# Kernel tuning notes

Measured on AMD Instinct MI355X. Metric: run time of the kernel, lower is better.

The kernel has to match this reference:

```python
import jax, jax.numpy as jnp
import numpy as np

N, DEG, F, H, OUT = 50000, 16, 128, 128, 64


def _lstm_aggr(neigh, w_ih, w_hh, b_ih, b_hh):
    # neigh: [N, D, F] fixed-degree neighbor features; run LSTM over D steps,
    # return final hidden state [N, H] (PyG SAGEConv 'lstm' aggregation).
    n, d, f = neigh.shape
    h_dim = w_hh.shape[1]

    def step(carry, xt):
        h, c = carry
        gates = xt @ w_ih.T + b_ih + h @ w_hh.T + b_hh  # [N, 4H]
        i, fg, g, o = jnp.split(gates, 4, axis=-1)      # torch gate order i,f,g,o
        i = jax.nn.sigmoid(i)
        fg = jax.nn.sigmoid(fg)
        g = jnp.tanh(g)
        o = jax.nn.sigmoid(o)
        c = fg * c + i * g
        h = o * jnp.tanh(c)
        return (h, c), None

    h0 = jnp.zeros((n, h_dim), neigh.dtype)
    (h, _), _ = jax.lax.scan(step, (h0, h0), jnp.swapaxes(neigh, 0, 1))
    return h


def _sage_lstm(x, src, w_ih, w_hh, b_ih, b_hh, wl, bl, wr):
    # SAGEConv: out = lin_l(lstm_aggr(x[neighbors])) + lin_r(x)
    neigh = x[src]                                   # [N, D, F] gather
    aggr = _lstm_aggr(neigh, w_ih, w_hh, b_ih, b_hh)  # [N, H]
    return aggr @ wl.T + bl + x @ wr.T


def setup_inputs() -> dict:
    key = jax.random.key(0)
    ks = jax.random.split(key, 16)
    x = jax.random.normal(ks[0], (N, F), dtype=jnp.float32)
    # fixed-degree graph: dst = arange(N) each repeated DEG times (sorted, as
    # PyG lstm aggregation requires), src random -> edge_index [2, N*DEG]
    src = jax.random.randint(ks[1], (N * DEG,), 0, N, dtype=jnp.int64)
    dst = jnp.repeat(jnp.arange(N, dtype=jnp.int64), DEG)
    edge_index = jnp.stack([src, dst])
    s = 1.0 / np.sqrt(H)
    def u(k, shape):
        return jax.random.uniform(k, shape, jnp.float32, -s, s)
    params = {
        # layer 1 (input F -> hidden H)
        "w_ih1": u(ks[2], (4 * H, F)), "w_hh1": u(ks[3], (4 * H, H)),
        "b_ih1": u(ks[4], (4 * H,)), "b_hh1": u(ks[5], (4 * H,)),
        "lin_l1_w": u(ks[6], (H, H)), "lin_l1_b": u(ks[6], (H,)),
        "lin_r1_w": u(ks[7], (H, F)),
        # layer 2 (H -> H)
        "w_ih2": u(ks[8], (4 * H, H)), "w_hh2": u(ks[9], (4 * H, H)),
        "b_ih2": u(ks[10], (4 * H,)), "b_hh2": u(ks[11], (4 * H,)),
        "lin_l2_w": u(ks[12], (H, H)), "lin_l2_b": u(ks[12], (H,)),
        "lin_r2_w": u(ks[13], (H, H)),
        # output head
        "lin_w": u(ks[14], (OUT, H)), "lin_b": u(ks[15], (OUT,)),
    }
    return {"x": x, "edge_index": edge_index, **params}


def reference(x, edge_index,
              w_ih1, w_hh1, b_ih1, b_hh1, lin_l1_w, lin_l1_b, lin_r1_w,
              w_ih2, w_hh2, b_ih2, b_hh2, lin_l2_w, lin_l2_b, lin_r2_w,
              lin_w, lin_b):
    n = x.shape[0]
    deg = edge_index.shape[1] // n
    src = edge_index[0].reshape(n, deg)  # fixed-degree neighbor matrix
    h = _sage_lstm(x, src, w_ih1, w_hh1, b_ih1, b_hh1, lin_l1_w, lin_l1_b, lin_r1_w)
    h = jax.nn.relu(h)
    h = _sage_lstm(h, src, w_ih2, w_hh2, b_ih2, b_hh2, lin_l2_w, lin_l2_b, lin_r2_w)
    h = jax.nn.relu(h)
    return h @ lin_w.T + lin_b
```

## Files before the change

### kernel.cpp

```cpp
#include <hip/hip_runtime.h>
#include <stdint.h>

#define NN 50000
#define DEG 16
#define MT 32
#define NBLK ((NN + MT - 1) / MT)
#define LOG2E 1.4426950408889634f

typedef short bf16x8 __attribute__((ext_vector_type(8)));
typedef float f32x4 __attribute__((ext_vector_type(4)));
typedef unsigned short u16;
typedef unsigned int u32;

static __device__ __forceinline__ u16 f2bf(float f) {
  union { float f; u32 u; } v; v.f = f;
  u32 u = v.u + 0x7FFFu + ((v.u >> 16) & 1u);
  return (u16)(u >> 16);
}
static __device__ __forceinline__ float rcp_(float x) {
  return __builtin_amdgcn_rcpf(x);
}
static __device__ __forceinline__ float ex2_(float x) {
  return __builtin_amdgcn_exp2f(x);
}
static __device__ __forceinline__ void gload_lds16(const void* g, void* l) {
  __builtin_amdgcn_global_load_lds(
      (const __attribute__((address_space(1))) void*)g,
      (__attribute__((address_space(3))) void*)l, 16, 0, 0);
}

__global__ void k_prep(const float* __restrict__ x, u16* __restrict__ xb,
                       const float* __restrict__ wih1, const float* __restrict__ whh1, u16* __restrict__ wpk1,
                       const float* __restrict__ wih2, const float* __restrict__ whh2, u16* __restrict__ wpk2,
                       const float* __restrict__ lr1, const float* __restrict__ ll1, u16* __restrict__ epk1,
                       const float* __restrict__ lr2, const float* __restrict__ ll2, u16* __restrict__ epk2,
                       const float* __restrict__ linw, u16* __restrict__ hpk,
                       const float* __restrict__ bi1, const float* __restrict__ bh1, float* __restrict__ bs1,
                       const float* __restrict__ bi2, const float* __restrict__ bh2, float* __restrict__ bs2) {
  int b = blockIdx.x;
  if (b < 128) {
    const float* wih = (b < 64) ? wih1 : wih2;
    const float* whh = (b < 64) ? whh1 : whh2;
    u16* wpk = (b < 64) ? wpk1 : wpk2;
    int t = (b & 63) * 256 + threadIdx.x;
    int lane = t & 63, kt = (t >> 6) & 7, g = (t >> 9) & 3, w = (t >> 11) & 7;
    int col = g * 128 + w * 16 + (lane & 15);
    int k0 = kt * 32 + (lane >> 4) * 8;
    float sc = (g == 2) ? 2.f * LOG2E : LOG2E;
#pragma unroll
    for (int j = 0; j < 8; ++j) {
      int k = k0 + j;
      float v = (k < 128) ? wih[col * 128 + k] : whh[col * 128 + k - 128];
      wpk[t * 8 + j] = f2bf(sc * v);
    }
  } else if (b < 160) {
    const float* lrw = (b < 144) ? lr1 : lr2;
    const float* llw = (b < 144) ? ll1 : ll2;
    u16* epk = (b < 144) ? epk1 : epk2;
    int t = ((b - 128) & 15) * 256 + threadIdx.x;
    int lane = t & 63, kt = (t >> 6) & 7, w = (t >> 9) & 7;
    int col = w * 16 + (lane & 15);
    int k0 = kt * 32 + (lane >> 4) * 8;
#pragma unroll
    for (int j = 0; j < 8; ++j) {
      int k = k0 + j;
      epk[t * 8 + j] = f2bf(k < 128 ? lrw[col * 128 + k] : llw[col * 128 + k - 128]);
    }
  } else if (b < 164) {
    int t = (b - 160) * 256 + threadIdx.x;
    int lane = t & 63, kt = (t >> 6) & 3, w = (t >> 8) & 3;
    int col = w * 16 + (lane & 15);
    int k0 = kt * 32 + (lane >> 4) * 8;
#pragma unroll
    for (int j = 0; j < 8; ++j) hpk[t * 8 + j] = f2bf(linw[col * 128 + k0 + j]);
  } else if (b < 168) {
    int t = (b - 164) * 256 + threadIdx.x;
    if (t < 1024) {
      int i = t & 511;
      float sc = ((i >> 7) == 2) ? 2.f * LOG2E : LOG2E;
      if (t < 512) bs1[i] = sc * (bi1[i] + bh1[i]);
      else bs2[i] = sc * (bi2[i] + bh2[i]);
    }
  } else {
    int i = (b - 168) * 256 + threadIdx.x;
    int stride = (gridDim.x - 168) * 256;
    for (; i < NN * 128 / 4; i += stride) {
      float4 v = ((const float4*)x)[i];
      ushort4 o;
      o.x = f2bf(v.x); o.y = f2bf(v.y); o.z = f2bf(v.z); o.w = f2bf(v.w);
      ((ushort4*)xb)[i] = o;
    }
  }
}


#define GATHER(DCODE, PDST)                                                   \
  do {                                                                        \
    int idx_;                                                                 \
    if ((DCODE) < DEG) idx_ = IDX[grow * DEG + (DCODE)];                      \
    else idx_ = (node0 + grow < NN) ? node0 + grow : NN - 1;                  \
    const char* gsw_ = (const char*)(xin + (size_t)idx_ * 128) +              \
                       ((lr * 16) ^ ((grow & 15) << 4));                      \
    gload_lds16(gsw_, (PDST) + (w * 4) * 128);                                \
  } while (0)

#define CBAR(N)                                                               \
  do {                                                                        \
    asm volatile("s_waitcnt vmcnt(" #N ") lgkmcnt(0)" ::: "memory");          \
    __builtin_amdgcn_s_barrier();                                             \
    __builtin_amdgcn_sched_barrier(0);                                        \
  } while (0)

template <int L2>
__global__ __launch_bounds__(512, 2) void k_layer(
    const u16* __restrict__ xin, const int* __restrict__ src,
    const u16* __restrict__ wpk, const float* __restrict__ bsum,
    const u16* __restrict__ epk, const float* __restrict__ linlb,
    u16* __restrict__ hout, const u16* __restrict__ hpk,
    const float* __restrict__ linb, float* __restrict__ dout) {
  __shared__ __align__(16) u16 AX[3][MT * 128];
  __shared__ __align__(16) u16 AH[2][MT * 128];
  __shared__ int IDX[MT * DEG];

  const int tid = threadIdx.x;
  const int w = tid >> 6, l = tid & 63;
  const int lr = l & 15, lh = l >> 4;
  const int node0 = blockIdx.x * MT;
  const int grow = w * 4 + lh;

  bf16x8 wreg[4][8];
#pragma unroll
  for (int g = 0; g < 4; ++g)
#pragma unroll
    for (int kt = 0; kt < 8; ++kt)
      wreg[g][kt] = *(const bf16x8*)(wpk + (size_t)(((w * 4 + g) * 8 + kt) * 64 + l) * 8);

  IDX[tid] = (node0 + (tid >> 4) < NN) ? src[node0 * DEG + tid] : 0;

  float gb[4];
#pragma unroll
  for (int g = 0; g < 4; ++g) gb[g] = bsum[g * 128 + w * 16 + lr];
  float eb = linlb[w * 16 + lr];
  __syncthreads();

  GATHER(0, AX[0]);
  GATHER(1, AX[1]);

  f32x4 c[2];
  c[0] = (f32x4){0.f, 0.f, 0.f, 0.f};
  c[1] = (f32x4){0.f, 0.f, 0.f, 0.f};
  CBAR(1);

  u16 *pA = AX[0], *pB = AX[1], *pC = AX[2];

#pragma unroll 1
  for (int step = 0; step < DEG; ++step) {
    const int cb = step & 1, nb = cb ^ 1;

    if (step < DEG - 1) GATHER(step + 2, pC);

    f32x4 acc[2][4];
#pragma unroll
    for (int mt = 0; mt < 2; ++mt)
#pragma unroll
      for (int g = 0; g < 4; ++g)
        acc[mt][g] = (f32x4){gb[g], gb[g], gb[g], gb[g]};

#pragma unroll
    for (int kt = 0; kt < 4; ++kt) {
      bf16x8 af[2];
#pragma unroll
      for (int mt = 0; mt < 2; ++mt) {
        int row = mt * 16 + lr;
        af[mt] = *(const bf16x8*)((const char*)pA + row * 256 +
                                  ((kt * 64 + lh * 16) ^ ((row & 15) << 4)));
      }
#pragma unroll
      for (int g = 0; g < 4; ++g)
#pragma unroll
        for (int mt = 0; mt < 2; ++mt)
          acc[mt][g] = __builtin_amdgcn_mfma_f32_16x16x32_bf16(af[mt], wreg[g][kt], acc[mt][g], 0, 0, 0);
    }

    if (step) {
#pragma unroll
      for (int kt = 0; kt < 4; ++kt) {
        bf16x8 af[2];
#pragma unroll
        for (int mt = 0; mt < 2; ++mt) {
          int row = mt * 16 + lr;
          af[mt] = *(const bf16x8*)((const char*)AH[cb] + row * 256 +
                                    ((kt * 64 + lh * 16) ^ ((row & 15) << 4)));
        }
#pragma unroll
        for (int g = 0; g < 4; ++g)
#pragma unroll
          for (int mt = 0; mt < 2; ++mt)
            acc[mt][g] = __builtin_amdgcn_mfma_f32_16x16x32_bf16(af[mt], wreg[g][4 + kt], acc[mt][g], 0, 0, 0);
      }
    }

#pragma unroll
    for (int mt = 0; mt < 2; ++mt)
#pragma unroll
      for (int r = 0; r < 4; ++r) {
        float iv = rcp_(1.f + ex2_(-acc[mt][0][r]));
        float fv = rcp_(1.f + ex2_(-acc[mt][1][r]));
        float gv = 1.f - 2.f * rcp_(1.f + ex2_(acc[mt][2][r]));
        float ov = rcp_(1.f + ex2_(-acc[mt][3][r]));
        float cv = fv * c[mt][r] + iv * gv;
        c[mt][r] = cv;
        float th = 1.f - 2.f * rcp_(1.f + ex2_(2.f * LOG2E * cv));
        int row = mt * 16 + lh * 4 + r;
        int jj = 2 * (w * 16 + lr);
        *(u16*)((char*)AH[nb] + row * 256 + (jj ^ ((row & 15) << 4))) =
            f2bf(ov * th);
      }

    if (step < DEG - 1) CBAR(1);
    else CBAR(0);

    u16* t_ = pA; pA = pB; pB = t_; 
    t_ = pB; pB = pC; pC = t_;
  }

  f32x4 eacc[2];
  eacc[0] = (f32x4){eb, eb, eb, eb};
  eacc[1] = (f32x4){eb, eb, eb, eb};
#pragma unroll
  for (int kt = 0; kt < 8; ++kt) {
    const u16* srcb = (kt < 4) ? pA : AH[0];
    int kb = (kt & 3) * 64 + lh * 16;
    bf16x8 af[2];
#pragma unroll
    for (int mt = 0; mt < 2; ++mt) {
      int row = mt * 16 + lr;
      af[mt] = *(const bf16x8*)((const char*)srcb + row * 256 +
                                (kb ^ ((row & 15) << 4)));
    }
    bf16x8 bf = *(const bf16x8*)(epk + (size_t)((w * 8 + kt) * 64 + l) * 8);
#pragma unroll
    for (int mt = 0; mt < 2; ++mt)
      eacc[mt] = __builtin_amdgcn_mfma_f32_16x16x32_bf16(af[mt], bf, eacc[mt], 0, 0, 0);
  }

  if constexpr (!L2) {
#pragma unroll
    for (int mt = 0; mt < 2; ++mt)
#pragma unroll
      for (int r = 0; r < 4; ++r) {
        int node = node0 + mt * 16 + lh * 4 + r;
        if (node < NN) {
          float v = fmaxf(eacc[mt][r], 0.f);
          hout[(size_t)node * 128 + w * 16 + lr] = f2bf(v);
        }
      }
  } else {
#pragma unroll
    for (int mt = 0; mt < 2; ++mt)
#pragma unroll
      for (int r = 0; r < 4; ++r) {
        int row = mt * 16 + lh * 4 + r;
        float v = fmaxf(eacc[mt][r], 0.f);
        int jj = 2 * (w * 16 + lr);
        *(u16*)((char*)AH[1] + row * 256 + (jj ^ ((row & 15) << 4))) = f2bf(v);
      }
    __syncthreads();
    if (w < 4) {
      float hb = linb[w * 16 + lr];
      f32x4 hacc[2];
      hacc[0] = (f32x4){hb, hb, hb, hb};
      hacc[1] = (f32x4){hb, hb, hb, hb};
#pragma unroll
      for (int kt = 0; kt < 4; ++kt) {
        bf16x8 af[2];
#pragma unroll
        for (int mt = 0; mt < 2; ++mt) {
          int row = mt * 16 + lr;
          af[mt] = *(const bf16x8*)((const char*)AH[1] + row * 256 +
                                    ((kt * 64 + lh * 16) ^ ((row & 15) << 4)));
        }
        bf16x8 bf = *(const bf16x8*)(hpk + (size_t)((w * 4 + kt) * 64 + l) * 8);
#pragma unroll
        for (int mt = 0; mt < 2; ++mt)
          hacc[mt] = __builtin_amdgcn_mfma_f32_16x16x32_bf16(af[mt], bf, hacc[mt], 0, 0, 0);
      }
#pragma unroll
      for (int mt = 0; mt < 2; ++mt)
#pragma unroll
        for (int r = 0; r < 4; ++r) {
          int node = node0 + mt * 16 + lh * 4 + r;
          if (node < NN) dout[(size_t)node * 64 + w * 16 + lr] = hacc[mt][r];
        }
    }
  }
}

extern "C" void kernel_launch(void* const* d_in, const int* in_sizes, int n_in,
                              void* d_out, int out_size, void* d_ws, size_t ws_size,
                              hipStream_t stream) {
  const float* x    = (const float*)d_in[0];
  const int*   edge = (const int*)d_in[1];
  const float* wih1 = (const float*)d_in[2];
  const float* whh1 = (const float*)d_in[3];
  const float* bih1 = (const float*)d_in[4];
  const float* bhh1 = (const float*)d_in[5];
  const float* ll1w = (const float*)d_in[6];
  const float* ll1b = (const float*)d_in[7];
  const float* lr1w = (const float*)d_in[8];
  const float* wih2 = (const float*)d_in[9];
  const float* whh2 = (const float*)d_in[10];
  const float* bih2 = (const float*)d_in[11];
  const float* bhh2 = (const float*)d_in[12];
  const float* ll2w = (const float*)d_in[13];
  const float* ll2b = (const float*)d_in[14];
  const float* lr2w = (const float*)d_in[15];
  const float* linw = (const float*)d_in[16];
  const float* linb = (const float*)d_in[17];

  char* ws = (char*)d_ws;
  u16* xb    = (u16*)(ws);
  u16* h1b   = (u16*)(ws + 12800000);
  u16* wpk1  = (u16*)(ws + 25600000);
  u16* wpk2  = (u16*)(ws + 25862144);
  u16* epk1  = (u16*)(ws + 26124288);
  u16* epk2  = (u16*)(ws + 26189824);
  u16* hpk   = (u16*)(ws + 26255360);
  float* bs1 = (float*)(ws + 26271744);
  float* bs2 = (float*)(ws + 26273792);

  k_prep<<<1000, 256, 0, stream>>>(x, xb,
                                   wih1, whh1, wpk1, wih2, whh2, wpk2,
                                   lr1w, ll1w, epk1, lr2w, ll2w, epk2,
                                   linw, hpk,
                                   bih1, bhh1, bs1, bih2, bhh2, bs2);
  k_layer<0><<<NBLK, 512, 0, stream>>>(xb, edge, wpk1, bs1, epk1, ll1b,
                                       h1b, nullptr, nullptr, nullptr);
  k_layer<1><<<NBLK, 512, 0, stream>>>(h1b, edge, wpk2, bs2, epk2, ll2b,
                                       nullptr, hpk, linb, (float*)d_out);
}
```

Baseline: 530.0 us.

## Load gathered neighbor rows directly into registers with 16-node tiles

Reduces the node tile from 32 to 16 rows per block. Gathered neighbor features now go straight from global memory into MFMA operand registers instead of through a triple-buffered LDS staging area. The input-projection MFMAs for the next step are interleaved with the recurrent step, and s_setprio is added around MFMA bursts. This drops LDS traffic and the vmcnt waits, and doubles the block count for occupancy and latency hiding. In exchange each block has more barrier and per-step overhead and reuses each weight-register load over half as many rows. The bounds checks are removed because 50000 divides evenly by 16.

```diff
diff --git a/kernel.cpp b/kernel.cpp
--- a/kernel.cpp
+++ b/kernel.cpp
@@ -3,7 +3,7 @@
 
 #define NN 50000
 #define DEG 16
-#define MT 32
+#define MT 16
 #define NBLK ((NN + MT - 1) / MT)
 #define LOG2E 1.4426950408889634f
 
@@ -22,11 +22,6 @@
 }
 static __device__ __forceinline__ float ex2_(float x) {
   return __builtin_amdgcn_exp2f(x);
-}
-static __device__ __forceinline__ void gload_lds16(const void* g, void* l) {
-  __builtin_amdgcn_global_load_lds(
-      (const __attribute__((address_space(1))) void*)g,
-      (__attribute__((address_space(3))) void*)l, 16, 0, 0);
 }
 
 __global__ void k_prep(const float* __restrict__ x, u16* __restrict__ xb,
@@ -94,19 +89,30 @@
 }
 
 
-#define GATHER(DCODE, PDST)                                                   \
+#define XLOAD(DCODE)                                                          \
   do {                                                                        \
-    int idx_;                                                                 \
-    if ((DCODE) < DEG) idx_ = IDX[grow * DEG + (DCODE)];                      \
-    else idx_ = (node0 + grow < NN) ? node0 + grow : NN - 1;                  \
-    const char* gsw_ = (const char*)(xin + (size_t)idx_ * 128) +              \
-                       ((lr * 16) ^ ((grow & 15) << 4));                      \
-    gload_lds16(gsw_, (PDST) + (w * 4) * 128);                                \
+    int idx_ = ((DCODE) < DEG) ? IDXT[(DCODE) * 16 + lr] : node0 + lr;        \
+    const u16* b_ = xin + (size_t)idx_ * 128 + lh * 8;                        \
+    xf[0] = *(const bf16x8*)(b_);                                             \
+    xf[1] = *(const bf16x8*)(b_ + 32);                                        \
+    xf[2] = *(const bf16x8*)(b_ + 64);                                        \
+    xf[3] = *(const bf16x8*)(b_ + 96);                                        \
   } while (0)
 
-#define CBAR(N)                                                               \
+#define XPART()                                                               \
   do {                                                                        \
-    asm volatile("s_waitcnt vmcnt(" #N ") lgkmcnt(0)" ::: "memory");          \
+    __builtin_amdgcn_s_setprio(1);                                            \
+    _Pragma("unroll") for (int g = 0; g < 4; ++g)                             \
+        acc[g] = (f32x4){gb[g], gb[g], gb[g], gb[g]};                         \
+    _Pragma("unroll") for (int kt = 0; kt < 4; ++kt)                          \
+        _Pragma("unroll") for (int g = 0; g < 4; ++g)                         \
+            acc[g] = __builtin_amdgcn_mfma_f32_16x16x32_bf16(xf[kt], wreg[g][kt], acc[g], 0, 0, 0); \
+    __builtin_amdgcn_s_setprio(0);                                            \
+  } while (0)
+
+#define EBAR()                                                                \
+  do {                                                                        \
+    asm volatile("s_waitcnt lgkmcnt(0)" ::: "memory");                        \
     __builtin_amdgcn_s_barrier();                                             \
     __builtin_amdgcn_sched_barrier(0);                                        \
   } while (0)
@@ -118,15 +124,13 @@
     const u16* __restrict__ epk, const float* __restrict__ linlb,
     u16* __restrict__ hout, const u16* __restrict__ hpk,
     const float* __restrict__ linb, float* __restrict__ dout) {
-  __shared__ __align__(16) u16 AX[3][MT * 128];
   __shared__ __align__(16) u16 AH[2][MT * 128];
-  __shared__ int IDX[MT * DEG];
+  __shared__ int IDXT[DEG * MT];
 
   const int tid = threadIdx.x;
   const int w = tid >> 6, l = tid & 63;
   const int lr = l & 15, lh = l >> 4;
   const int node0 = blockIdx.x * MT;
-  const int grow = w * 4 + lh;
 
   bf16x8 wreg[4][8];
 #pragma unroll
@@ -135,7 +139,9 @@
     for (int kt = 0; kt < 8; ++kt)
       wreg[g][kt] = *(const bf16x8*)(wpk + (size_t)(((w * 4 + g) * 8 + kt) * 64 + l) * 8);
 
-  IDX[tid] = (node0 + (tid >> 4) < NN) ? src[node0 * DEG + tid] : 0;
+  if (tid < MT * DEG) {
+    IDXT[(tid & 15) * 16 + (tid >> 4)] = src[node0 * DEG + tid];
+  }
 
   float gb[4];
 #pragma unroll
@@ -143,155 +149,99 @@
   float eb = linlb[w * 16 + lr];
   __syncthreads();
 
-  GATHER(0, AX[0]);
-  GATHER(1, AX[1]);
-
-  f32x4 c[2];
-  c[0] = (f32x4){0.f, 0.f, 0.f, 0.f};
-  c[1] = (f32x4){0.f, 0.f, 0.f, 0.f};
-  CBAR(1);
-
-  u16 *pA = AX[0], *pB = AX[1], *pC = AX[2];
+  bf16x8 xf[4];
+  f32x4 acc[4];
+  f32x4 c4 = (f32x4){0.f, 0.f, 0.f, 0.f};
+
+  XLOAD(0);
+  XPART();
+  XLOAD(1);
 
 #pragma unroll 1
   for (int step = 0; step < DEG; ++step) {
     const int cb = step & 1, nb = cb ^ 1;
 
-    if (step < DEG - 1) GATHER(step + 2, pC);
-
-    f32x4 acc[2][4];
-#pragma unroll
-    for (int mt = 0; mt < 2; ++mt)
-#pragma unroll
-      for (int g = 0; g < 4; ++g)
-        acc[mt][g] = (f32x4){gb[g], gb[g], gb[g], gb[g]};
-
-#pragma unroll
-    for (int kt = 0; kt < 4; ++kt) {
-      bf16x8 af[2];
-#pragma unroll
-      for (int mt = 0; mt < 2; ++mt) {
-        int row = mt * 16 + lr;
-        af[mt] = *(const bf16x8*)((const char*)pA + row * 256 +
-                                  ((kt * 64 + lh * 16) ^ ((row & 15) << 4)));
+    if (step) {
+      __builtin_amdgcn_s_setprio(1);
+#pragma unroll
+      for (int kt = 0; kt < 4; ++kt) {
+        bf16x8 af = *(const bf16x8*)((const char*)AH[cb] + lr * 256 +
+                                     ((kt * 64 + lh * 16) ^ ((lr & 15) << 4)));
+#pragma unroll
+        for (int g = 0; g < 4; ++g)
+          acc[g] = __builtin_amdgcn_mfma_f32_16x16x32_bf16(af, wreg[g][4 + kt], acc[g], 0, 0, 0);
       }
-#pragma unroll
-      for (int g = 0; g < 4; ++g)
-#pragma unroll
-        for (int mt = 0; mt < 2; ++mt)
-          acc[mt][g] = __builtin_amdgcn_mfma_f32_16x16x32_bf16(af[mt], wreg[g][kt], acc[mt][g], 0, 0, 0);
-    }
-
-    if (step) {
-#pragma unroll
-      for (int kt = 0; kt < 4; ++kt) {
-        bf16x8 af[2];
-#pragma unroll
-        for (int mt = 0; mt < 2; ++mt) {
-          int row = mt * 16 + lr;
-          af[mt] = *(const bf16x8*)((const char*)AH[cb] + row * 256 +
-                                    ((kt * 64 + lh * 16) ^ ((row & 15) << 4)));
-        }
-#pragma unroll
-        for (int g = 0; g < 4; ++g)
-#pragma unroll
-          for (int mt = 0; mt < 2; ++mt)
-            acc[mt][g] = __builtin_amdgcn_mfma_f32_16x16x32_bf16(af[mt], wreg[g][4 + kt], acc[mt][g], 0, 0, 0);
-      }
-    }
-
-#pragma unroll
-    for (int mt = 0; mt < 2; ++mt)
-#pragma unroll
-      for (int r = 0; r < 4; ++r) {
-        float iv = rcp_(1.f + ex2_(-acc[mt][0][r]));
-        float fv = rcp_(1.f + ex2_(-acc[mt][1][r]));
-        float gv = 1.f - 2.f * rcp_(1.f + ex2_(acc[mt][2][r]));
-        float ov = rcp_(1.f + ex2_(-acc[mt][3][r]));
-        float cv = fv * c[mt][r] + iv * gv;
-        c[mt][r] = cv;
-        float th = 1.f - 2.f * rcp_(1.f + ex2_(2.f * LOG2E * cv));
-        int row = mt * 16 + lh * 4 + r;
-        int jj = 2 * (w * 16 + lr);
-        *(u16*)((char*)AH[nb] + row * 256 + (jj ^ ((row & 15) << 4))) =
-            f2bf(ov * th);
-      }
-
-    if (step < DEG - 1) CBAR(1);
-    else CBAR(0);
-
-    u16* t_ = pA; pA = pB; pB = t_; 
-    t_ = pB; pB = pC; pC = t_;
-  }
-
-  f32x4 eacc[2];
-  eacc[0] = (f32x4){eb, eb, eb, eb};
-  eacc[1] = (f32x4){eb, eb, eb, eb};
-#pragma unroll
-  for (int kt = 0; kt < 8; ++kt) {
-    const u16* srcb = (kt < 4) ? pA : AH[0];
-    int kb = (kt & 3) * 64 + lh * 16;
-    bf16x8 af[2];
-#pragma unroll
-    for (int mt = 0; mt < 2; ++mt) {
-      int row = mt * 16 + lr;
-      af[mt] = *(const bf16x8*)((const char*)srcb + row * 256 +
-                                (kb ^ ((row & 15) << 4)));
-    }
+      __builtin_amdgcn_s_setprio(0);
+    }
+
+#pragma unroll
+    for (int r = 0; r < 4; ++r) {
+      float iv = rcp_(1.f + ex2_(-acc[0][r]));
+      float fv = rcp_(1.f + ex2_(-acc[1][r]));
+      float gv = 1.f - 2.f * rcp_(1.f + ex2_(acc[2][r]));
+      float ov = rcp_(1.f + ex2_(-acc[3][r]));
+      float cv = fv * c4[r] + iv * gv;
+      c4[r] = cv;
+      float th = 1.f - 2.f * rcp_(1.f + ex2_(2.f * LOG2E * cv));
+      int row = lh * 4 + r;
+      int jj = 2 * (w * 16 + lr);
+      *(u16*)((char*)AH[nb] + row * 256 + (jj ^ ((row & 15) << 4))) =
+          f2bf(ov * th);
+    }
+
+    if (step < DEG - 1) {
+      XPART();
+      XLOAD(step + 2);
+    }
+
+    EBAR();
+  }
+
+  f32x4 eacc = (f32x4){eb, eb, eb, eb};
+#pragma unroll
+  for (int kt = 0; kt < 4; ++kt) {
     bf16x8 bf = *(const bf16x8*)(epk + (size_t)((w * 8 + kt) * 64 + l) * 8);
-#pragma unroll
-    for (int mt = 0; mt < 2; ++mt)
-      eacc[mt] = __builtin_amdgcn_mfma_f32_16x16x32_bf16(af[mt], bf, eacc[mt], 0, 0, 0);
+    eacc = __builtin_amdgcn_mfma_f32_16x16x32_bf16(xf[kt], bf, eacc, 0, 0, 0);
+  }
+#pragma unroll
+  for (int kt = 0; kt < 4; ++kt) {
+    bf16x8 af = *(const bf16x8*)((const char*)AH[0] + lr * 256 +
+                                 ((kt * 64 + lh * 16) ^ ((lr & 15) << 4)));
+    bf16x8 bf = *(const bf16x8*)(epk + (size_t)((w * 8 + 4 + kt) * 64 + l) * 8);
+    eacc = __builtin_amdgcn_mfma_f32_16x16x32_bf16(af, bf, eacc, 0, 0, 0);
   }
 
   if constexpr (!L2) {
 #pragma unroll
-    for (int mt = 0; mt < 2; ++mt)
-#pragma unroll
-      for (int r = 0; r < 4; ++r) {
-        int node = node0 + mt * 16 + lh * 4 + r;
-        if (node < NN) {
-          float v = fmaxf(eacc[mt][r], 0.f);
-          hout[(size_t)node * 128 + w * 16 + lr] = f2bf(v);
-        }
-      }
+    for (int r = 0; r < 4; ++r) {
+      int node = node0 + lh * 4 + r;
+      float v = fmaxf(eacc[r], 0.f);
+      hout[(size_t)node * 128 + w * 16 + lr] = f2bf(v);
+    }
   } else {
 #pragma unroll
-    for (int mt = 0; mt < 2; ++mt)
-#pragma unroll
-      for (int r = 0; r < 4; ++r) {
-        int row = mt * 16 + lh * 4 + r;
-        float v = fmaxf(eacc[mt][r], 0.f);
-        int jj = 2 * (w * 16 + lr);
-        *(u16*)((char*)AH[1] + row * 256 + (jj ^ ((row & 15) << 4))) = f2bf(v);
-      }
+    for (int r = 0; r < 4; ++r) {
+      int row = lh * 4 + r;
+      float v = fmaxf(eacc[r], 0.f);
+      int jj = 2 * (w * 16 + lr);
+      *(u16*)((char*)AH[1] + row * 256 + (jj ^ ((row & 15) << 4))) = f2bf(v);
+    }
     __syncthreads();
     if (w < 4) {
       float hb = linb[w * 16 + lr];
-      f32x4 hacc[2];
-      hacc[0] = (f32x4){hb, hb, hb, hb};
-      hacc[1] = (f32x4){hb, hb, hb, hb};
+      f32x4 hacc = (f32x4){hb, hb, hb, hb};
 #pragma unroll
       for (int kt = 0; kt < 4; ++kt) {
-        bf16x8 af[2];
-#pragma unroll
-        for (int mt = 0; mt < 2; ++mt) {
-          int row = mt * 16 + lr;
-          af[mt] = *(const bf16x8*)((const char*)AH[1] + row * 256 +
-                                    ((kt * 64 + lh * 16) ^ ((row & 15) << 4)));
-        }
+        bf16x8 af = *(const bf16x8*)((const char*)AH[1] + lr * 256 +
+                                     ((kt * 64 + lh * 16) ^ ((lr & 15) << 4)));
         bf16x8 bf = *(const bf16x8*)(hpk + (size_t)((w * 4 + kt) * 64 + l) * 8);
-#pragma unroll
-        for (int mt = 0; mt < 2; ++mt)
-          hacc[mt] = __builtin_amdgcn_mfma_f32_16x16x32_bf16(af[mt], bf, hacc[mt], 0, 0, 0);
+        hacc = __builtin_amdgcn_mfma_f32_16x16x32_bf16(af, bf, hacc, 0, 0, 0);
       }
 #pragma unroll
-      for (int mt = 0; mt < 2; ++mt)
-#pragma unroll
-        for (int r = 0; r < 4; ++r) {
-          int node = node0 + mt * 16 + lh * 4 + r;
-          if (node < NN) dout[(size_t)node * 64 + w * 16 + lr] = hacc[mt][r];
-        }
+      for (int r = 0; r < 4; ++r) {
+        int node = node0 + lh * 4 + r;
+        dout[(size_t)node * 64 + w * 16 + lr] = hacc[r];
+      }
     }
   }
 }
```

Measured after the change: 563.1 us. +6.2%, slower.
